# Kernel optimization log

Measured on AMD Instinct MI355X. Metric: run time of the kernel, lower is better.

The kernel has to match this reference:

```python
import jax, jax.numpy as jnp
import numpy as np

N_ROWS = 4_194_304  # batch rows
N_LAYERS = 30


def setup_inputs() -> dict:
    key = jax.random.key(0)
    k1, k2, k3, k4, k5 = jax.random.split(key, 5)
    x1 = jax.random.normal(k1, (N_ROWS, 1), dtype=jnp.float32)
    x2 = jax.random.normal(k2, (N_ROWS, 5), dtype=jnp.float32)
    # Per-layer params stacked: Linear(5->1) weight [1,5] + bias [1]; Linear(1->5, no bias) weight [5,1]
    W1 = jax.random.normal(k3, (N_LAYERS, 1, 5), dtype=jnp.float32) * (1.0 / np.sqrt(5.0))
    b1 = jax.random.normal(k4, (N_LAYERS, 1), dtype=jnp.float32) * (1.0 / np.sqrt(5.0))
    W2 = jax.random.normal(k5, (N_LAYERS, 5, 1), dtype=jnp.float32)
    return {"x1": x1, "x2": x2, "W1": W1, "b1": b1, "W2": W2}


def reference(x1, x2, W1, b1, W2):
    # Chain of 30 UpDownDoubleResNetBlock blocks:
    #   x1 = x1 + relu(x2) @ W1^T + b1   (Linear(5,1) with bias)
    #   x2 = x2 + relu(x1) @ W2^T        (Linear(1,5) no bias)
    def step(carry, params):
        h1, h2 = carry
        w1, bb1, w2 = params  # [1,5], [1], [5,1]
        h1 = h1 + jax.nn.relu(h2) @ w1.T + bb1  # [N,1]
        h2 = h2 + jax.nn.relu(h1) @ w2.T        # [N,5]
        return (h1, h2), None

    (x1, x2), _ = jax.lax.scan(step, (x1, x2), (W1, b1, W2))
    return (x1, x2)
```

## Files before the change

kernel.cpp:

```cpp
#include <hip/hip_runtime.h>

#define NL 30

__global__ __launch_bounds__(256) void drn_kernel(
    const float* __restrict__ x1, const float* __restrict__ x2,
    const float* __restrict__ W1, const float* __restrict__ b1,
    const float* __restrict__ W2,
    float* __restrict__ o1, float* __restrict__ o2, int nrows)
{
    __shared__ __align__(16) float sp[NL * 12];
    for (int i = threadIdx.x; i < NL * 12; i += blockDim.x) {
        int l = i / 12, k = i % 12;
        float v = 0.0f;
        if (k < 5)        v = W1[l * 5 + k];
        else if (k == 5)  v = b1[l];
        else if (k < 11)  v = W2[l * 5 + (k - 6)];
        sp[i] = v;
    }
    __syncthreads();

    long t = (long)blockIdx.x * blockDim.x + threadIdx.x;
    long row0 = t * 4;
    if (row0 >= nrows) return;

    float h1[4];
    float h2[20];
    *(float4*)&h1[0] = *(const float4*)(x1 + row0);
    const float4* px2 = (const float4*)(x2 + row0 * 5);
    #pragma unroll
    for (int i = 0; i < 5; ++i) ((float4*)h2)[i] = px2[i];

    for (int l = 0; l < NL; ++l) {
        float4 p0 = *(const float4*)&sp[l * 12];
        float4 p1 = *(const float4*)&sp[l * 12 + 4];
        float4 p2 = *(const float4*)&sp[l * 12 + 8];
        float w1r[5] = {p0.x, p0.y, p0.z, p0.w, p1.x};
        float bb     = p1.y;
        float w2r[5] = {p1.z, p1.w, p2.x, p2.y, p2.z};
        #pragma unroll
        for (int r = 0; r < 4; ++r) {
            float s = bb;
            #pragma unroll
            for (int j = 0; j < 5; ++j)
                s = fmaf(fmaxf(h2[r * 5 + j], 0.0f), w1r[j], s);
            h1[r] += s;
            float rh = fmaxf(h1[r], 0.0f);
            #pragma unroll
            for (int j = 0; j < 5; ++j)
                h2[r * 5 + j] = fmaf(rh, w2r[j], h2[r * 5 + j]);
        }
    }

    *(float4*)(o1 + row0) = *(float4*)&h1[0];
    float4* po2 = (float4*)(o2 + row0 * 5);
    #pragma unroll
    for (int i = 0; i < 5; ++i) po2[i] = ((float4*)h2)[i];
}

extern "C" void kernel_launch(void* const* d_in, const int* in_sizes, int n_in,
                              void* d_out, int out_size, void* d_ws, size_t ws_size,
                              hipStream_t stream) {
    const float* x1 = (const float*)d_in[0];
    const float* x2 = (const float*)d_in[1];
    const float* W1 = (const float*)d_in[2];
    const float* b1 = (const float*)d_in[3];
    const float* W2 = (const float*)d_in[4];
    int nrows = in_sizes[0];
    float* o1 = (float*)d_out;
    float* o2 = (float*)d_out + nrows;

    int nthreads = nrows / 4;
    int block = 256;
    int grid = (nthreads + block - 1) / block;
    drn_kernel<<<grid, block, 0, stream>>>(x1, x2, W1, b1, W2, o1, o2, nrows);
}
```

Measured before the change: 205.0 us.

## Use packed f32x2 math across row pairs and read weights directly from global

```diff
diff --git a/kernel.cpp b/kernel.cpp
--- a/kernel.cpp
+++ b/kernel.cpp
@@ -1,6 +1,10 @@
 #include <hip/hip_runtime.h>
 
 #define NL 30
+
+typedef float f32x2 __attribute__((ext_vector_type(2)));
+
+static __device__ __forceinline__ f32x2 splat2(float v) { return (f32x2){v, v}; }
 
 __global__ __launch_bounds__(256) void drn_kernel(
     const float* __restrict__ x1, const float* __restrict__ x2,
@@ -8,53 +12,63 @@
     const float* __restrict__ W2,
     float* __restrict__ o1, float* __restrict__ o2, int nrows)
 {
-    __shared__ __align__(16) float sp[NL * 12];
-    for (int i = threadIdx.x; i < NL * 12; i += blockDim.x) {
-        int l = i / 12, k = i % 12;
-        float v = 0.0f;
-        if (k < 5)        v = W1[l * 5 + k];
-        else if (k == 5)  v = b1[l];
-        else if (k < 11)  v = W2[l * 5 + (k - 6)];
-        sp[i] = v;
-    }
-    __syncthreads();
-
     long t = (long)blockIdx.x * blockDim.x + threadIdx.x;
     long row0 = t * 4;
     if (row0 >= nrows) return;
 
-    float h1[4];
-    float h2[20];
-    *(float4*)&h1[0] = *(const float4*)(x1 + row0);
-    const float4* px2 = (const float4*)(x2 + row0 * 5);
+    float4 h1v = *(const float4*)(x1 + row0);
+    float xs[20];
+    {
+        const float4* px2 = (const float4*)(x2 + row0 * 5);
+        #pragma unroll
+        for (int i = 0; i < 5; ++i) ((float4*)xs)[i] = px2[i];
+    }
+
+    f32x2 h1p[2] = { (f32x2){h1v.x, h1v.y}, (f32x2){h1v.z, h1v.w} };
+    f32x2 h2[5][2];
     #pragma unroll
-    for (int i = 0; i < 5; ++i) ((float4*)h2)[i] = px2[i];
+    for (int j = 0; j < 5; ++j) {
+        h2[j][0] = (f32x2){xs[0 * 5 + j], xs[1 * 5 + j]};
+        h2[j][1] = (f32x2){xs[2 * 5 + j], xs[3 * 5 + j]};
+    }
+
+    const f32x2 zero = splat2(0.0f);
 
     for (int l = 0; l < NL; ++l) {
-        float4 p0 = *(const float4*)&sp[l * 12];
-        float4 p1 = *(const float4*)&sp[l * 12 + 4];
-        float4 p2 = *(const float4*)&sp[l * 12 + 8];
-        float w1r[5] = {p0.x, p0.y, p0.z, p0.w, p1.x};
-        float bb     = p1.y;
-        float w2r[5] = {p1.z, p1.w, p2.x, p2.y, p2.z};
+        float w1r[5], w2r[5];
         #pragma unroll
-        for (int r = 0; r < 4; ++r) {
-            float s = bb;
+        for (int j = 0; j < 5; ++j) w1r[j] = W1[l * 5 + j];
+        float bb = b1[l];
+        #pragma unroll
+        for (int j = 0; j < 5; ++j) w2r[j] = W2[l * 5 + j];
+
+        #pragma unroll
+        for (int p = 0; p < 2; ++p) {
+            f32x2 s = h1p[p] + splat2(bb);
             #pragma unroll
             for (int j = 0; j < 5; ++j)
-                s = fmaf(fmaxf(h2[r * 5 + j], 0.0f), w1r[j], s);
-            h1[r] += s;
-            float rh = fmaxf(h1[r], 0.0f);
+                s += __builtin_elementwise_max(h2[j][p], zero) * splat2(w1r[j]);
+            h1p[p] = s;
+            f32x2 rh = __builtin_elementwise_max(s, zero);
             #pragma unroll
             for (int j = 0; j < 5; ++j)
-                h2[r * 5 + j] = fmaf(rh, w2r[j], h2[r * 5 + j]);
+                h2[j][p] += rh * splat2(w2r[j]);
         }
     }
 
-    *(float4*)(o1 + row0) = *(float4*)&h1[0];
+    float ys[20];
+    #pragma unroll
+    for (int j = 0; j < 5; ++j) {
+        ys[0 * 5 + j] = h2[j][0].x;
+        ys[1 * 5 + j] = h2[j][0].y;
+        ys[2 * 5 + j] = h2[j][1].x;
+        ys[3 * 5 + j] = h2[j][1].y;
+    }
+
+    *(float4*)(o1 + row0) = make_float4(h1p[0].x, h1p[0].y, h1p[1].x, h1p[1].y);
     float4* po2 = (float4*)(o2 + row0 * 5);
     #pragma unroll
-    for (int i = 0; i < 5; ++i) po2[i] = ((float4*)h2)[i];
+    for (int i = 0; i < 5; ++i) po2[i] = ((float4*)ys)[i];
 }
 
 extern "C" void kernel_launch(void* const* d_in, const int* in_sizes, int n_in,
```

Result: no change. 206.9 us (+0.9%).

## Use packed float2 math with two rows per thread and pre-packed params

Applied to the files above, without the earlier changes.

```diff
diff --git a/kernel.cpp b/kernel.cpp
--- a/kernel.cpp
+++ b/kernel.cpp
@@ -2,59 +2,74 @@
 
 #define NL 30
 
-__global__ __launch_bounds__(256) void drn_kernel(
+typedef float f2 __attribute__((ext_vector_type(2)));
+
+__global__ void pack_params(const float* __restrict__ W1,
+                            const float* __restrict__ b1,
+                            const float* __restrict__ W2,
+                            f2* __restrict__ pw) {
+    int i = blockIdx.x * blockDim.x + threadIdx.x;
+    if (i >= NL * 12) return;
+    int l = i / 12, k = i % 12;
+    float v = 0.0f;
+    if (k < 5)       v = W1[l * 5 + k];
+    else if (k == 5) v = b1[l];
+    else if (k < 11) v = W2[l * 5 + (k - 6)];
+    pw[i] = (f2){v, v};
+}
+
+__global__ __launch_bounds__(256, 8) void drn_kernel(
     const float* __restrict__ x1, const float* __restrict__ x2,
-    const float* __restrict__ W1, const float* __restrict__ b1,
-    const float* __restrict__ W2,
-    float* __restrict__ o1, float* __restrict__ o2, int nrows)
+    const f2* __restrict__ pw,
+    float* __restrict__ o1, float* __restrict__ o2)
 {
-    __shared__ __align__(16) float sp[NL * 12];
-    for (int i = threadIdx.x; i < NL * 12; i += blockDim.x) {
-        int l = i / 12, k = i % 12;
-        float v = 0.0f;
-        if (k < 5)        v = W1[l * 5 + k];
-        else if (k == 5)  v = b1[l];
-        else if (k < 11)  v = W2[l * 5 + (k - 6)];
-        sp[i] = v;
-    }
-    __syncthreads();
+    long row = ((long)blockIdx.x * 256 + threadIdx.x) * 2;
 
-    long t = (long)blockIdx.x * blockDim.x + threadIdx.x;
-    long row0 = t * 4;
-    if (row0 >= nrows) return;
-
-    float h1[4];
-    float h2[20];
-    *(float4*)&h1[0] = *(const float4*)(x1 + row0);
-    const float4* px2 = (const float4*)(x2 + row0 * 5);
-    #pragma unroll
-    for (int i = 0; i < 5; ++i) ((float4*)h2)[i] = px2[i];
-
-    for (int l = 0; l < NL; ++l) {
-        float4 p0 = *(const float4*)&sp[l * 12];
-        float4 p1 = *(const float4*)&sp[l * 12 + 4];
-        float4 p2 = *(const float4*)&sp[l * 12 + 8];
-        float w1r[5] = {p0.x, p0.y, p0.z, p0.w, p1.x};
-        float bb     = p1.y;
-        float w2r[5] = {p1.z, p1.w, p2.x, p2.y, p2.z};
-        #pragma unroll
-        for (int r = 0; r < 4; ++r) {
-            float s = bb;
-            #pragma unroll
-            for (int j = 0; j < 5; ++j)
-                s = fmaf(fmaxf(h2[r * 5 + j], 0.0f), w1r[j], s);
-            h1[r] += s;
-            float rh = fmaxf(h1[r], 0.0f);
-            #pragma unroll
-            for (int j = 0; j < 5; ++j)
-                h2[r * 5 + j] = fmaf(rh, w2r[j], h2[r * 5 + j]);
-        }
+    f2 h1 = *(const f2*)(x1 + row);
+    f2 h2[5];
+    {
+        const f2* p = (const f2*)(x2 + row * 5);
+        f2 a0 = p[0], a1 = p[1], a2 = p[2], a3 = p[3], a4 = p[4];
+        h2[0] = (f2){a0.x, a2.y};
+        h2[1] = (f2){a0.y, a3.x};
+        h2[2] = (f2){a1.x, a3.y};
+        h2[3] = (f2){a1.y, a4.x};
+        h2[4] = (f2){a2.x, a4.y};
     }
 
-    *(float4*)(o1 + row0) = *(float4*)&h1[0];
-    float4* po2 = (float4*)(o2 + row0 * 5);
+    const f2 zero = (f2){0.0f, 0.0f};
+
     #pragma unroll
-    for (int i = 0; i < 5; ++i) po2[i] = ((float4*)h2)[i];
+    for (int l = 0; l < NL; ++l) {
+        const f2* P = pw + l * 12;
+        f2 w1d[5], w2d[5], bd;
+        #pragma unroll
+        for (int j = 0; j < 5; ++j) w1d[j] = P[j];
+        bd = P[5];
+        #pragma unroll
+        for (int j = 0; j < 5; ++j) w2d[j] = P[6 + j];
+
+        f2 s = h1 + bd;
+        #pragma unroll
+        for (int j = 0; j < 5; ++j)
+            s = __builtin_elementwise_fma(__builtin_elementwise_max(h2[j], zero),
+                                          w1d[j], s);
+        h1 = s;
+        f2 rh = __builtin_elementwise_max(s, zero);
+        #pragma unroll
+        for (int j = 0; j < 5; ++j)
+            h2[j] = __builtin_elementwise_fma(rh, w2d[j], h2[j]);
+    }
+
+    *(f2*)(o1 + row) = h1;
+    {
+        f2* p = (f2*)(o2 + row * 5);
+        p[0] = (f2){h2[0].x, h2[1].x};
+        p[1] = (f2){h2[2].x, h2[3].x};
+        p[2] = (f2){h2[4].x, h2[0].y};
+        p[3] = (f2){h2[1].y, h2[2].y};
+        p[4] = (f2){h2[3].y, h2[4].y};
+    }
 }
 
 extern "C" void kernel_launch(void* const* d_in, const int* in_sizes, int n_in,
@@ -68,9 +83,11 @@
     int nrows = in_sizes[0];
     float* o1 = (float*)d_out;
     float* o2 = (float*)d_out + nrows;
+    f2* pw = (f2*)d_ws;
 
-    int nthreads = nrows / 4;
+    pack_params<<<2, 256, 0, stream>>>(W1, b1, W2, pw);
+
     int block = 256;
-    int grid = (nthreads + block - 1) / block;
-    drn_kernel<<<grid, block, 0, stream>>>(x1, x2, W1, b1, W2, o1, o2, nrows);
+    int grid = nrows / (block * 2);
+    drn_kernel<<<grid, block, 0, stream>>>(x1, x2, pw, o1, o2);
 }
```

Result: faster. 196.6 us (-4.1%).
